# Optimization experiments

Measured on AMD Instinct MI355X. Metric: run time of the kernel, lower is better.

Reference implementation:

```python
import jax, jax.numpy as jnp
import numpy as np

N_NODES = 50000
N_EDGES = 800000
NODE_F = 100     # memory_feats
EDGE_F = 100     # raw edge feature dim
TIME_D = 100     # temporal encoder dimension
HEADS = 2
OUT_F = 100
NEG_SLOPE = 0.2


def setup_inputs() -> dict:
    key = jax.random.key(0)
    ks = jax.random.split(key, 16)
    return {
        'memory': jax.random.normal(ks[0], (N_NODES, NODE_F), jnp.float32),
        'node_ts': jax.random.uniform(ks[1], (N_NODES,), jnp.float32),
        'edge_feats_raw': jax.random.normal(ks[2], (N_EDGES, EDGE_F), jnp.float32),
        'edge_ts': jax.random.uniform(ks[3], (N_EDGES,), jnp.float32),
        'time_w': jax.random.normal(ks[4], (TIME_D,), jnp.float32),
        'time_b': jax.random.normal(ks[5], (TIME_D,), jnp.float32),
        'fc_node_w': jax.random.normal(ks[6], (NODE_F, HEADS * OUT_F), jnp.float32) * 0.1,
        'fc_node_b': jax.random.normal(ks[7], (HEADS * OUT_F,), jnp.float32) * 0.1,
        'fc_edge_w': jax.random.normal(ks[8], (EDGE_F + TIME_D, HEADS * OUT_F), jnp.float32) * 0.1,
        'fc_edge_b': jax.random.normal(ks[9], (HEADS * OUT_F,), jnp.float32) * 0.1,
        'attn_l': jax.random.normal(ks[10], (HEADS, OUT_F), jnp.float32) * 0.1,
        'attn_r': jax.random.normal(ks[11], (HEADS, OUT_F), jnp.float32) * 0.1,
        'attn_e': jax.random.normal(ks[12], (HEADS, OUT_F), jnp.float32) * 0.1,
        'src': jax.random.randint(ks[13], (N_EDGES,), 0, N_NODES, jnp.int32),
        'dst': jax.random.randint(ks[14], (N_EDGES,), 0, N_NODES, jnp.int32),
    }


def _forward(memory, node_ts, edge_feats_raw, edge_ts,
             time_w, time_b, fc_node_w, fc_node_b, fc_edge_w, fc_edge_b,
             attn_l, attn_r, attn_e, src, dst):
    n = memory.shape[0]
    # TemporalEdgePreprocess: Fourier time encoding of (edge_ts - ts[src])
    time_diff = edge_ts - node_ts[src]                                  # [E]
    te = jnp.cos(time_diff[:, None] * time_w[None, :] + time_b[None, :])  # [E, T]
    efeat = jnp.concatenate([edge_feats_raw, te], axis=1)               # [E, EDGE_F+T]

    # EdgeGATConv (eval mode: dropouts are identity)
    node_feat = (memory @ fc_node_w + fc_node_b).reshape(n, HEADS, OUT_F)          # [N,H,F]
    edge_feat = (efeat @ fc_edge_w + fc_edge_b).reshape(-1, HEADS, OUT_F)          # [E,H,F]

    el = jnp.einsum('nhf,hf->nh', node_feat, attn_l)   # [N,H]
    er = jnp.einsum('nhf,hf->nh', node_feat, attn_r)   # [N,H]
    ee = jnp.einsum('ehf,hf->eh', edge_feat, attn_e)   # [E,H]

    el_prime = el[src] + ee                             # u_add_e  [E,H]
    e = el_prime + er[dst]                              # e_add_v  [E,H]
    e = jnp.where(e > 0, e, NEG_SLOPE * e)              # leaky_relu

    # edge_softmax: softmax over incoming edges per destination node, per head
    emax = jax.ops.segment_max(e, dst, num_segments=n)  # [N,H]
    emax = jnp.where(jnp.isfinite(emax), emax, 0.0)     # zero-in-degree safety
    e_exp = jnp.exp(e - emax[dst])                      # [E,H]
    denom = jax.ops.segment_sum(e_exp, dst, num_segments=n)  # [N,H]
    a = e_exp / denom[dst]                              # [E,H]

    # msg_fn: m = a * el_prime (el_prime has singleton feature dim in torch code)
    m = a * el_prime                                    # [E,H]
    ft = jax.ops.segment_sum(m, dst, num_segments=n)    # [N,H]  (== [N,H,1] features)

    # residual: Identity since memory_feats == out_feats -> view(N,-1,F) = [N,1,F]
    rst = ft[:, :, None] + memory[:, None, :]           # [N,H,F] via broadcast
    return rst.mean(axis=1)                             # .mean(1) over heads -> [N,F]


def reference(memory, node_ts, edge_feats_raw, edge_ts,
              time_w, time_b, fc_node_w, fc_node_b, fc_edge_w, fc_edge_b,
              attn_l, attn_r, attn_e, src, dst):
    return _forward(memory, node_ts, edge_feats_raw, edge_ts,
                    time_w, time_b, fc_node_w, fc_node_b, fc_edge_w, fc_edge_b,
                    attn_l, attn_r, attn_e, src, dst)
```

## Files before the change

kernel.cpp:

```cpp
#include <hip/hip_runtime.h>


constexpr int F = 100;
constexpr float NEG_SLOPE = 0.2f;
constexpr int EPB = 32;
constexpr int NREP = 8;

__device__ __forceinline__ float wave_reduce(float v) {
#pragma unroll
    for (int off = 32; off > 0; off >>= 1)
        v += __shfl_down(v, off, 64);
    return v;
}

__global__ void precompute_kernel(
    const float* __restrict__ fc_node_w, const float* __restrict__ fc_node_b,
    const float* __restrict__ fc_edge_w, const float* __restrict__ fc_edge_b,
    const float* __restrict__ attn_l, const float* __restrict__ attn_r,
    const float* __restrict__ attn_e,
    float4* __restrict__ w_node, float2* __restrict__ w_edge,
    float* __restrict__ bias)
{
    int wid  = blockIdx.x * (blockDim.x >> 6) + (threadIdx.x >> 6);
    int lane = threadIdx.x & 63;
    if (wid < F) {
        int t = wid;
        float a0 = 0.f, a1 = 0.f, a2 = 0.f, a3 = 0.f;
        for (int f = lane; f < F; f += 64) {
            float w0 = fc_node_w[t * 2 * F + f];
            float w1 = fc_node_w[t * 2 * F + F + f];
            a0 += w0 * attn_l[f];
            a1 += w1 * attn_l[F + f];
            a2 += w0 * attn_r[f];
            a3 += w1 * attn_r[F + f];
        }
        a0 = wave_reduce(a0); a1 = wave_reduce(a1);
        a2 = wave_reduce(a2); a3 = wave_reduce(a3);
        if (lane == 0) w_node[t] = make_float4(a0, a1, a2, a3);
    } else if (wid < 3 * F) {
        int t = wid - F;
        float a0 = 0.f, a1 = 0.f;
        for (int f = lane; f < F; f += 64) {
            a0 += fc_edge_w[t * 2 * F + f] * attn_e[f];
            a1 += fc_edge_w[t * 2 * F + F + f] * attn_e[F + f];
        }
        a0 = wave_reduce(a0); a1 = wave_reduce(a1);
        if (lane == 0) w_edge[t] = make_float2(a0, a1);
    } else if (wid < 3 * F + 6) {
        int j = wid - 3 * F;
        const float* b  = (j < 4) ? fc_node_b : fc_edge_b;
        const float* av = (j < 2) ? attn_l : (j < 4 ? attn_r : attn_e);
        int h = j & 1;
        float a0 = 0.f;
        for (int f = lane; f < F; f += 64)
            a0 += b[h * F + f] * av[h * F + f];
        a0 = wave_reduce(a0);
        if (lane == 0) bias[j] = a0;
    }
}

__global__ void node_kernel(const float* __restrict__ memory,
                            const float4* __restrict__ w_node,
                            const float* __restrict__ bias,
                            float4* __restrict__ el_er, int N)
{
    int n    = blockIdx.x * (blockDim.x >> 6) + (threadIdx.x >> 6);
    int lane = threadIdx.x & 63;
    if (n >= N) return;
    const float* mrow = memory + (size_t)n * F;
    float a0 = 0.f, a1 = 0.f, a2 = 0.f, a3 = 0.f;
    for (int k = lane; k < F; k += 64) {
        float m  = mrow[k];
        float4 w = w_node[k];
        a0 += m * w.x; a1 += m * w.y; a2 += m * w.z; a3 += m * w.w;
    }
    a0 = wave_reduce(a0); a1 = wave_reduce(a1);
    a2 = wave_reduce(a2); a3 = wave_reduce(a3);
    if (lane == 0)
        el_er[n] = make_float4(a0 + bias[0], a1 + bias[1],
                               a2 + bias[2], a3 + bias[3]);
}

__global__ void zero_kernel(float4* __restrict__ acc, int n4)
{
    int i = blockIdx.x * blockDim.x + threadIdx.x;
    if (i < n4) acc[i] = make_float4(0.f, 0.f, 0.f, 0.f);
}

__global__ void edge_gemv_kernel(
    const float* __restrict__ edge_raw,
    const float* __restrict__ edge_ts,
    const float* __restrict__ node_ts,
    const int* __restrict__ src,
    const int* __restrict__ dst,
    const float* __restrict__ time_w,
    const float* __restrict__ time_b,
    const float2* __restrict__ w_edge,
    const float* __restrict__ bias,
    const float4* __restrict__ el_er,
    float4* __restrict__ edge_y, int E)
{
    __shared__ float4 wx4[25], wy4[25], wz4[25], ww4[25], tw4[25], tb4[25];
    __shared__ float  td_s[EPB];
    __shared__ float2 el_s[EPB];
    __shared__ float2 er_s[EPB];

    const int  t  = threadIdx.x;
    const long eb = (long)blockIdx.x * EPB;

    if (t < 25) {
        float4 x, y, z, w, tw, tb;
#pragma unroll
        for (int j = 0; j < 4; ++j) {
            int k = 4 * t + j;
            float2 wr = w_edge[k];
            float2 wt = w_edge[F + k];
            ((float*)&x)[j]  = wr.x;  ((float*)&y)[j]  = wr.y;
            ((float*)&z)[j]  = wt.x;  ((float*)&w)[j]  = wt.y;
            ((float*)&tw)[j] = time_w[k];
            ((float*)&tb)[j] = time_b[k];
        }
        wx4[t] = x; wy4[t] = y; wz4[t] = z; ww4[t] = w;
        tw4[t] = tw; tb4[t] = tb;
    } else if (t >= 64 && t < 64 + EPB) {
        int  l = t - 64;
        long e = eb + l;
        if (e < E) {
            int s = src[e], d = dst[e];
            td_s[l] = edge_ts[e] - node_ts[s];
            float4 a = el_er[s];
            float4 b = el_er[d];
            el_s[l] = make_float2(a.x, a.y);
            er_s[l] = make_float2(b.z, b.w);
        }
    }
    __syncthreads();

    const int  el_ = t >> 3;
    const int  s8  = t & 7;
    const long e   = eb + el_;
    float a0 = 0.f, a1 = 0.f;
    if (e < E) {
        const float  td   = td_s[el_];
        const float4* row = (const float4*)edge_raw + e * 25;
#pragma unroll
        for (int i = 0; i < 4; ++i) {
            int c = s8 + 8 * i;
            if (c < 25) {
                float4 r  = row[c];
                float4 x  = wx4[c], y = wy4[c], z = wz4[c], w = ww4[c];
                float4 tw = tw4[c], tb = tb4[c];
                float c0 = __cosf(fmaf(td, tw.x, tb.x));
                float c1 = __cosf(fmaf(td, tw.y, tb.y));
                float c2 = __cosf(fmaf(td, tw.z, tb.z));
                float c3 = __cosf(fmaf(td, tw.w, tb.w));
                a0 = fmaf(r.x, x.x, fmaf(c0, z.x, a0));
                a1 = fmaf(r.x, y.x, fmaf(c0, w.x, a1));
                a0 = fmaf(r.y, x.y, fmaf(c1, z.y, a0));
                a1 = fmaf(r.y, y.y, fmaf(c1, w.y, a1));
                a0 = fmaf(r.z, x.z, fmaf(c2, z.z, a0));
                a1 = fmaf(r.z, y.z, fmaf(c2, w.z, a1));
                a0 = fmaf(r.w, x.w, fmaf(c3, z.w, a0));
                a1 = fmaf(r.w, y.w, fmaf(c3, w.w, a1));
            }
        }
    }
    a0 += __shfl_down(a0, 4, 64);  a1 += __shfl_down(a1, 4, 64);
    a0 += __shfl_down(a0, 2, 64);  a1 += __shfl_down(a1, 2, 64);
    a0 += __shfl_down(a0, 1, 64);  a1 += __shfl_down(a1, 1, 64);

    if (s8 == 0 && e < E) {
        float elp0 = el_s[el_].x + a0 + bias[4];
        float elp1 = el_s[el_].y + a1 + bias[5];
        float e0 = elp0 + er_s[el_].x;
        float e1 = elp1 + er_s[el_].y;
        e0 = e0 > 0.f ? e0 : NEG_SLOPE * e0;
        e1 = e1 > 0.f ? e1 : NEG_SLOPE * e1;
        float x0 = __expf(e0);
        float x1 = __expf(e1);
        edge_y[e] = make_float4(x0 * elp0, x1 * elp1, x0, x1);
    }
}

__global__ void scatter_kernel(const float4* __restrict__ edge_y,
                               const int* __restrict__ dst,
                               float* __restrict__ acc, int E, int N)
{
    int i = blockIdx.x * blockDim.x + threadIdx.x;
    if (i >= E) return;
    float4 y = edge_y[i];
    int d = dst[i];
    int r = threadIdx.x & (NREP - 1);
    float* a = acc + ((size_t)r * N + d) * 4;
    atomicAdd(a + 0, y.x);
    atomicAdd(a + 1, y.y);
    atomicAdd(a + 2, y.z);
    atomicAdd(a + 3, y.w);
}

__global__ void finalize_kernel(const float4* __restrict__ acc,
                                float* __restrict__ addbuf, int N)
{
    int n = blockIdx.x * blockDim.x + threadIdx.x;
    if (n >= N) return;
    float s0 = 0.f, s1 = 0.f, s2 = 0.f, s3 = 0.f;
#pragma unroll
    for (int r = 0; r < NREP; ++r) {
        float4 v = acc[(size_t)r * N + n];
        s0 += v.x; s1 += v.y; s2 += v.z; s3 += v.w;
    }
    float ft0 = (s2 != 0.f) ? s0 / s2 : 0.f;
    float ft1 = (s3 != 0.f) ? s1 / s3 : 0.f;
    addbuf[n] = 0.5f * (ft0 + ft1);
}

__global__ void out_kernel(const float* __restrict__ memory,
                           const float* __restrict__ addbuf,
                           float* __restrict__ out, int N)
{
    int i = blockIdx.x * blockDim.x + threadIdx.x;
    int total = N * (F / 2);
    if (i >= total) return;
    int n = i / (F / 2);
    float add = addbuf[n];
    float2 m = ((const float2*)memory)[i];
    float2 o;
    o.x = m.x + add;
    o.y = m.y + add;
    ((float2*)out)[i] = o;
}

extern "C" void kernel_launch(void* const* d_in, const int* in_sizes, int n_in,
                              void* d_out, int out_size, void* d_ws, size_t ws_size,
                              hipStream_t stream)
{
    const float* memory     = (const float*)d_in[0];
    const float* node_ts    = (const float*)d_in[1];
    const float* edge_raw   = (const float*)d_in[2];
    const float* edge_ts    = (const float*)d_in[3];
    const float* time_w     = (const float*)d_in[4];
    const float* time_b     = (const float*)d_in[5];
    const float* fc_node_w  = (const float*)d_in[6];
    const float* fc_node_b  = (const float*)d_in[7];
    const float* fc_edge_w  = (const float*)d_in[8];
    const float* fc_edge_b  = (const float*)d_in[9];
    const float* attn_l     = (const float*)d_in[10];
    const float* attn_r     = (const float*)d_in[11];
    const float* attn_e     = (const float*)d_in[12];
    const int*   src        = (const int*)d_in[13];
    const int*   dst        = (const int*)d_in[14];
    float*       out        = (float*)d_out;

    const int N = in_sizes[1];
    const int E = in_sizes[3];

    float* ws = (float*)d_ws;
    float4* w_node  = (float4*)ws;
    float2* w_edge  = (float2*)(ws + 400);
    float*  bias    = ws + 800;
    float4* el_er   = (float4*)(ws + 816);
    float4* acc     = (float4*)(ws + 816 + 4 * (size_t)N);
    float*  addbuf  = ws + 816 + 36 * (size_t)N;
    float4* edge_y  = (float4*)(ws + 816 + 37 * (size_t)N);

    {
        int waves  = 3 * F + 6;
        int blocks = (waves + 3) / 4;
        precompute_kernel<<<blocks, 256, 0, stream>>>(
            fc_node_w, fc_node_b, fc_edge_w, fc_edge_b,
            attn_l, attn_r, attn_e, w_node, w_edge, bias);
    }
    {
        int blocks = (N + 3) / 4;
        node_kernel<<<blocks, 256, 0, stream>>>(
            memory, w_node, bias, el_er, N);
    }
    {
        int n4     = NREP * N;
        int blocks = (n4 + 255) / 256;
        zero_kernel<<<blocks, 256, 0, stream>>>(acc, n4);
    }
    {
        int blocks = (E + EPB - 1) / EPB;
        edge_gemv_kernel<<<blocks, 256, 0, stream>>>(
            edge_raw, edge_ts, node_ts, src, dst, time_w, time_b,
            w_edge, bias, el_er, edge_y, E);
    }
    {
        int blocks = (E + 255) / 256;
        scatter_kernel<<<blocks, 256, 0, stream>>>(
            edge_y, dst, (float*)acc, E, N);
    }
    {
        int blocks = (N + 255) / 256;
        finalize_kernel<<<blocks, 256, 0, stream>>>(acc, addbuf, N);
    }
    {
        int total  = N * (F / 2);
        int blocks = (total + 255) / 256;
        out_kernel<<<blocks, 256, 0, stream>>>(memory, addbuf, out, N);
    }
}
```

Measured before the change: 650.5 us.

## Replace float atomic scatter with counting-sort buckets and segmented reduce

Replaces the replicated float atomic accumulation (8 replicas × 4 atomics per edge) with a counting sort by destination. Edges are counted per node and prefix-scanned into offsets, then the edge kernel writes its result into a per-destination bucket slot using one integer atomic. A reduce kernel sums each node's contiguous segment with 16 lanes. This trades four float atomics per edge for one int atomic plus extra count and scan passes, and the bucket writes land at scattered addresses.

```diff
diff --git a/kernel.cpp b/kernel.cpp
--- a/kernel.cpp
+++ b/kernel.cpp
@@ -4,7 +4,6 @@
 constexpr int F = 100;
 constexpr float NEG_SLOPE = 0.2f;
 constexpr int EPB = 32;
-constexpr int NREP = 8;
 
 __device__ __forceinline__ float wave_reduce(float v) {
 #pragma unroll
@@ -62,7 +61,8 @@
 __global__ void node_kernel(const float* __restrict__ memory,
                             const float4* __restrict__ w_node,
                             const float* __restrict__ bias,
-                            float4* __restrict__ el_er, int N)
+                            float4* __restrict__ el_er,
+                            int* __restrict__ cnt, int N)
 {
     int n    = blockIdx.x * (blockDim.x >> 6) + (threadIdx.x >> 6);
     int lane = threadIdx.x & 63;
@@ -79,12 +79,61 @@
     if (lane == 0)
         el_er[n] = make_float4(a0 + bias[0], a1 + bias[1],
                                a2 + bias[2], a3 + bias[3]);
-}
-
-__global__ void zero_kernel(float4* __restrict__ acc, int n4)
+    if (lane == 1)
+        cnt[n] = 0;
+}
+
+__global__ void count_kernel(const int* __restrict__ dst,
+                             int* __restrict__ cnt, int E)
 {
     int i = blockIdx.x * blockDim.x + threadIdx.x;
-    if (i < n4) acc[i] = make_float4(0.f, 0.f, 0.f, 0.f);
+    if (i < E) atomicAdd(&cnt[dst[i]], 1);
+}
+
+__global__ void scan1_kernel(const int* __restrict__ cnt,
+                             int* __restrict__ offs,
+                             int* __restrict__ bsum, int N)
+{
+    __shared__ int tmp[256];
+    int i = blockIdx.x * 256 + threadIdx.x;
+    int v = (i < N) ? cnt[i] : 0;
+    tmp[threadIdx.x] = v;
+    __syncthreads();
+    for (int d = 1; d < 256; d <<= 1) {
+        int t = (threadIdx.x >= d) ? tmp[threadIdx.x - d] : 0;
+        __syncthreads();
+        tmp[threadIdx.x] += t;
+        __syncthreads();
+    }
+    if (i < N) offs[i] = tmp[threadIdx.x] - v;
+    if (threadIdx.x == 255) bsum[blockIdx.x] = tmp[255];
+}
+
+__global__ void scan2_kernel(int* __restrict__ bsum, int nb)
+{
+    __shared__ int tmp[256];
+    int v = (threadIdx.x < nb) ? bsum[threadIdx.x] : 0;
+    tmp[threadIdx.x] = v;
+    __syncthreads();
+    for (int d = 1; d < 256; d <<= 1) {
+        int t = (threadIdx.x >= d) ? tmp[threadIdx.x - d] : 0;
+        __syncthreads();
+        tmp[threadIdx.x] += t;
+        __syncthreads();
+    }
+    if (threadIdx.x < nb) bsum[threadIdx.x] = tmp[threadIdx.x] - v;
+}
+
+__global__ void scan3_kernel(int* __restrict__ offs,
+                             const int* __restrict__ bsum,
+                             int* __restrict__ cursor, int N)
+{
+    int i = blockIdx.x * 256 + threadIdx.x;
+    if (i < N) {
+        int o = offs[i] + bsum[blockIdx.x];
+        offs[i]   = o;
+        cursor[i] = o;
+    }
 }
 
 __global__ void edge_gemv_kernel(
@@ -98,12 +147,14 @@
     const float2* __restrict__ w_edge,
     const float* __restrict__ bias,
     const float4* __restrict__ el_er,
-    float4* __restrict__ edge_y, int E)
+    int* __restrict__ cursor,
+    float4* __restrict__ bucket, int E)
 {
     __shared__ float4 wx4[25], wy4[25], wz4[25], ww4[25], tw4[25], tb4[25];
     __shared__ float  td_s[EPB];
     __shared__ float2 el_s[EPB];
     __shared__ float2 er_s[EPB];
+    __shared__ int    d_s[EPB];
 
     const int  t  = threadIdx.x;
     const long eb = (long)blockIdx.x * EPB;
@@ -127,6 +178,7 @@
         long e = eb + l;
         if (e < E) {
             int s = src[e], d = dst[e];
+            d_s[l]  = d;
             td_s[l] = edge_ts[e] - node_ts[s];
             float4 a = el_er[s];
             float4 b = el_er[d];
@@ -178,40 +230,39 @@
         e1 = e1 > 0.f ? e1 : NEG_SLOPE * e1;
         float x0 = __expf(e0);
         float x1 = __expf(e1);
-        edge_y[e] = make_float4(x0 * elp0, x1 * elp1, x0, x1);
-    }
-}
-
-__global__ void scatter_kernel(const float4* __restrict__ edge_y,
-                               const int* __restrict__ dst,
-                               float* __restrict__ acc, int E, int N)
-{
-    int i = blockIdx.x * blockDim.x + threadIdx.x;
-    if (i >= E) return;
-    float4 y = edge_y[i];
-    int d = dst[i];
-    int r = threadIdx.x & (NREP - 1);
-    float* a = acc + ((size_t)r * N + d) * 4;
-    atomicAdd(a + 0, y.x);
-    atomicAdd(a + 1, y.y);
-    atomicAdd(a + 2, y.z);
-    atomicAdd(a + 3, y.w);
-}
-
-__global__ void finalize_kernel(const float4* __restrict__ acc,
-                                float* __restrict__ addbuf, int N)
-{
-    int n = blockIdx.x * blockDim.x + threadIdx.x;
-    if (n >= N) return;
+        int pos = atomicAdd(&cursor[d_s[el_]], 1);
+        bucket[pos] = make_float4(x0 * elp0, x1 * elp1, x0, x1);
+    }
+}
+
+__global__ void reduce_kernel(const float4* __restrict__ bucket,
+                              const int* __restrict__ offs,
+                              const int* __restrict__ cnt,
+                              float* __restrict__ addbuf, int N)
+{
+    int g = blockIdx.x * (blockDim.x >> 4) + (threadIdx.x >> 4);
+    int l = threadIdx.x & 15;
+    if (g >= N) return;
+    int base = offs[g];
+    int deg  = cnt[g];
     float s0 = 0.f, s1 = 0.f, s2 = 0.f, s3 = 0.f;
-#pragma unroll
-    for (int r = 0; r < NREP; ++r) {
-        float4 v = acc[(size_t)r * N + n];
+    for (int j = l; j < deg; j += 16) {
+        float4 v = bucket[base + j];
         s0 += v.x; s1 += v.y; s2 += v.z; s3 += v.w;
     }
-    float ft0 = (s2 != 0.f) ? s0 / s2 : 0.f;
-    float ft1 = (s3 != 0.f) ? s1 / s3 : 0.f;
-    addbuf[n] = 0.5f * (ft0 + ft1);
+    s0 += __shfl_down(s0, 8, 64); s1 += __shfl_down(s1, 8, 64);
+    s2 += __shfl_down(s2, 8, 64); s3 += __shfl_down(s3, 8, 64);
+    s0 += __shfl_down(s0, 4, 64); s1 += __shfl_down(s1, 4, 64);
+    s2 += __shfl_down(s2, 4, 64); s3 += __shfl_down(s3, 4, 64);
+    s0 += __shfl_down(s0, 2, 64); s1 += __shfl_down(s1, 2, 64);
+    s2 += __shfl_down(s2, 2, 64); s3 += __shfl_down(s3, 2, 64);
+    s0 += __shfl_down(s0, 1, 64); s1 += __shfl_down(s1, 1, 64);
+    s2 += __shfl_down(s2, 1, 64); s3 += __shfl_down(s3, 1, 64);
+    if (l == 0) {
+        float ft0 = (s2 != 0.f) ? s0 / s2 : 0.f;
+        float ft1 = (s3 != 0.f) ? s1 / s3 : 0.f;
+        addbuf[g] = 0.5f * (ft0 + ft1);
+    }
 }
 
 __global__ void out_kernel(const float* __restrict__ memory,
@@ -259,9 +310,16 @@
     float2* w_edge  = (float2*)(ws + 400);
     float*  bias    = ws + 800;
     float4* el_er   = (float4*)(ws + 816);
-    float4* acc     = (float4*)(ws + 816 + 4 * (size_t)N);
-    float*  addbuf  = ws + 816 + 36 * (size_t)N;
-    float4* edge_y  = (float4*)(ws + 816 + 37 * (size_t)N);
+    float*  addbuf  = ws + 816 + 4 * (size_t)N;
+    int*    cnt     = (int*)(ws + 816 + 5 * (size_t)N);
+    int*    offs    = cnt + N;
+    int*    cursor  = offs + N;
+    int*    bsum    = cursor + N;
+    size_t  boff    = 816 + 8 * (size_t)N + 256;
+    boff            = (boff + 3) & ~(size_t)3;
+    float4* bucket  = (float4*)(ws + boff);
+
+    const int nb = (N + 255) / 256;
 
     {
         int waves  = 3 * F + 6;
@@ -273,27 +331,24 @@
     {
         int blocks = (N + 3) / 4;
         node_kernel<<<blocks, 256, 0, stream>>>(
-            memory, w_node, bias, el_er, N);
-    }
-    {
-        int n4     = NREP * N;
-        int blocks = (n4 + 255) / 256;
-        zero_kernel<<<blocks, 256, 0, stream>>>(acc, n4);
-    }
+            memory, w_node, bias, el_er, cnt, N);
+    }
+    {
+        int blocks = (E + 255) / 256;
+        count_kernel<<<blocks, 256, 0, stream>>>(dst, cnt, E);
+    }
+    scan1_kernel<<<nb, 256, 0, stream>>>(cnt, offs, bsum, N);
+    scan2_kernel<<<1, 256, 0, stream>>>(bsum, nb);
+    scan3_kernel<<<nb, 256, 0, stream>>>(offs, bsum, cursor, N);
     {
         int blocks = (E + EPB - 1) / EPB;
         edge_gemv_kernel<<<blocks, 256, 0, stream>>>(
             edge_raw, edge_ts, node_ts, src, dst, time_w, time_b,
-            w_edge, bias, el_er, edge_y, E);
-    }
-    {
-        int blocks = (E + 255) / 256;
-        scatter_kernel<<<blocks, 256, 0, stream>>>(
-            edge_y, dst, (float*)acc, E, N);
-    }
-    {
-        int blocks = (N + 255) / 256;
-        finalize_kernel<<<blocks, 256, 0, stream>>>(acc, addbuf, N);
+            w_edge, bias, el_er, cursor, bucket, E);
+    }
+    {
+        int blocks = (N + 15) / 16;
+        reduce_kernel<<<blocks, 256, 0, stream>>>(bucket, offs, cnt, addbuf, N);
     }
     {
         int total  = N * (F / 2);
```

New measurement: 551.0 us. 15.3% less time.
